# Kernel optimization log

Hardware: AMD Instinct MI355X
Metric: run time of the kernel (lower is better)

Reference implementation:

```python
import jax, jax.numpy as jnp
import numpy as np

B, N, S, D, K = 8, 8192, 2048, 256, 3
MLP = [256, 128]
EPS = 1e-5


def setup_inputs() -> dict:
    key = jax.random.key(0)
    ks = jax.random.split(key, 12)
    inp = {
        "xyz1": jax.random.normal(ks[0], (B, N, 3), dtype=jnp.float32),
        "xyz2": jax.random.normal(ks[1], (B, S, 3), dtype=jnp.float32),
        "points1": jax.random.normal(ks[2], (B, N, D), dtype=jnp.float32),
        "points2": jax.random.normal(ks[3], (B, S, D), dtype=jnp.float32),
        # relation conv: Conv2d(4 -> 1, kernel 1x1) == linear over last dim
        "rel_w": jax.random.normal(ks[4], (4,), dtype=jnp.float32) * 0.5,
        "rel_b": jnp.zeros((), dtype=jnp.float32),
        # mlp layer 0: Conv1d(2D -> 256, k=1) + BN
        "W0": jax.random.normal(ks[5], (MLP[0], 2 * D), dtype=jnp.float32) * (1.0 / np.sqrt(2 * D)),
        "b0": jnp.zeros((MLP[0],), dtype=jnp.float32),
        "g0": jnp.ones((MLP[0],), dtype=jnp.float32),
        "be0": jnp.zeros((MLP[0],), dtype=jnp.float32),
        # mlp layer 1: Conv1d(256 -> 128, k=1) + BN
        "W1": jax.random.normal(ks[6], (MLP[1], MLP[0]), dtype=jnp.float32) * (1.0 / np.sqrt(MLP[0])),
        "b1": jnp.zeros((MLP[1],), dtype=jnp.float32),
        "g1": jnp.ones((MLP[1],), dtype=jnp.float32),
        "be1": jnp.zeros((MLP[1],), dtype=jnp.float32),
    }
    return inp


def _gather(points, idx):
    # points: [B,S,C], idx: [B,N,K] -> [B,N,K,C]
    return jax.vmap(lambda p, i: p[i])(points, idx)


def _bn_relu(x, gamma, beta):
    # training-mode BatchNorm1d over [B,N,C]: stats over (B,N), biased var
    mean = jnp.mean(x, axis=(0, 1))
    var = jnp.var(x, axis=(0, 1))
    xn = (x - mean) * jax.lax.rsqrt(var + EPS)
    return jax.nn.relu(xn * gamma + beta)


def reference(xyz1, xyz2, points1, points2, rel_w, rel_b,
              W0, b0, g0, be0, W1, b1, g1, be1):
    # pairwise squared distances [B,N,S]
    d = (jnp.sum(xyz1 ** 2, -1)[:, :, None]
         + jnp.sum(xyz2 ** 2, -1)[:, None, :]
         - 2.0 * jnp.einsum('bnc,bmc->bnm', xyz1, xyz2))
    neg_d, idx = jax.lax.top_k(-d, K)          # K smallest distances
    dists = -neg_d                              # [B,N,K]

    offset = xyz1[:, :, None, :] - _gather(xyz2, idx)        # [B,N,K,3]
    rel = jnp.concatenate([dists[..., None], offset], -1)    # [B,N,K,4]
    weight = jax.nn.sigmoid(rel @ rel_w + rel_b)              # [B,N,K]

    interp = jnp.mean(_gather(points2, idx) * weight[..., None], axis=2)  # [B,N,D]
    h = jnp.concatenate([points1, interp], axis=-1)           # [B,N,2D]

    h = _bn_relu(jnp.einsum('bnc,oc->bno', h, W0) + b0, g0, be0)
    h = _bn_relu(jnp.einsum('bnc,oc->bno', h, W1) + b1, g1, be1)
    return h  # [B,N,128]
```

## Files before the change

### kernel.cpp

```cpp
#include <hip/hip_runtime.h>
#include <stdint.h>
#include <stddef.h>

#define B_   8
#define N_   8192
#define S_   2048
#define D_   256
#define M_   (B_*N_)
#define C0_  256
#define C1_  128
#define K2D_ 512
#define TS8_ 8
#define SEG8_ (S_/TS8_)
#define SWP_ 264

typedef __attribute__((ext_vector_type(8))) short short8;
typedef __attribute__((ext_vector_type(4))) float f32x4;
typedef __attribute__((ext_vector_type(2))) float f32x2;

__device__ __forceinline__ short f2bf(float f) {
  unsigned u = __float_as_uint(f);
  u += 0x7fffu + ((u >> 16) & 1u);
  return (short)(u >> 16);
}
__device__ __forceinline__ float bf2f(short s) {
  return __uint_as_float(((unsigned)(unsigned short)s) << 16);
}

__device__ __forceinline__ void cp16(const void* g, void* l) {
  __builtin_amdgcn_global_load_lds(
      (__attribute__((address_space(1))) void*)(g),
      (__attribute__((address_space(3))) void*)(l), 16, 0, 0);
}

__global__ void convw_kernel(const float* __restrict__ W0,
                             const float* __restrict__ W1,
                             const float* __restrict__ xyz2,
                             short* __restrict__ W0b, short* __restrict__ W1b,
                             float* __restrict__ xyz2p, float* __restrict__ stats) {
  int i = blockIdx.x * 256 + threadIdx.x;
  if (blockIdx.x == 0) {
    stats[threadIdx.x] = 0.f;
    stats[256 + threadIdx.x] = 0.f;
    stats[512 + threadIdx.x] = 0.f;
  }
  if (i < C0_ * K2D_) W0b[i] = f2bf(W0[i]);
  if (i < C1_ * C0_)  W1b[i] = f2bf(W1[i]);
  if (i < B_ * S_) {
    const int b = i >> 11, s = i & (S_ - 1);
    float x = xyz2[(size_t)i * 3 + 0];
    float y = xyz2[(size_t)i * 3 + 1];
    float z = xyz2[(size_t)i * 3 + 2];
    float ss = __fadd_rn(__fadd_rn(__fmul_rn(x, x), __fmul_rn(y, y)), __fmul_rn(z, z));
    float* xw = xyz2p + (size_t)b * 4 * S_;
    xw[s] = x; xw[S_ + s] = y; xw[2 * S_ + s] = z; xw[3 * S_ + s] = ss;
  }
}

__global__ __launch_bounds__(512, 8)
void topk_kernel(const float* __restrict__ xyz1, const float* __restrict__ xyz2p,
                 const float* __restrict__ relw, const float* __restrict__ relb,
                 int* __restrict__ idx_out, float* __restrict__ w_out) {
  __shared__ float cd[TS8_][64][3];
  __shared__ int   ci[TS8_][64][3];
  const int tid  = threadIdx.x;
  const int lane = tid & 63;
  const int seg  = __builtin_amdgcn_readfirstlane(tid >> 6);
  const int b    = blockIdx.x >> 7;
  const int n    = (blockIdx.x & 127) * 64 + lane;

  const float* p = xyz1 + ((size_t)b * N_ + n) * 3;
  const float ax = p[0], ay = p[1], az = p[2];
  const float s1 = __fadd_rn(__fadd_rn(__fmul_rn(ax, ax), __fmul_rn(ay, ay)), __fmul_rn(az, az));

  const float* xw = xyz2p + (size_t)b * 4 * S_;
  const f32x2* XP = (const f32x2*)(xw)           + seg * (SEG8_ / 2);
  const f32x2* YP = (const f32x2*)(xw + S_)      + seg * (SEG8_ / 2);
  const f32x2* ZP = (const f32x2*)(xw + 2 * S_)  + seg * (SEG8_ / 2);
  const f32x2* WP = (const f32x2*)(xw + 3 * S_)  + seg * (SEG8_ / 2);

  float d0 = 3.4e38f, d1 = 3.4e38f, d2 = 3.4e38f;
  int   i0 = 0, i1 = 0, i2 = 0;
  const int sbeg = seg * SEG8_;
  {
    #pragma clang fp contract(off)
    #pragma unroll 4
    for (int pr = 0; pr < SEG8_ / 2; pr++) {
      f32x2 X = XP[pr], Y = YP[pr], Z = ZP[pr], W = WP[pr];
      f32x2 t1 = ax * X;
      f32x2 t2 = ay * Y;
      f32x2 t3 = az * Z;
      f32x2 dt = (t1 + t2) + t3;
      f32x2 e  = s1 + W;
      f32x2 m  = 2.0f * dt;
      f32x2 d  = e - m;
      const float dlo = d.x, dhi = d.y;
      if (fminf(dlo, dhi) < d2) {
        const int s = sbeg + 2 * pr;
        if (dlo < d2) {
          if (dlo < d1) {
            d2 = d1; i2 = i1;
            if (dlo < d0) { d1 = d0; i1 = i0; d0 = dlo; i0 = s; }
            else          { d1 = dlo; i1 = s; }
          } else { d2 = dlo; i2 = s; }
        }
        if (dhi < d2) {
          if (dhi < d1) {
            d2 = d1; i2 = i1;
            if (dhi < d0) { d1 = d0; i1 = i0; d0 = dhi; i0 = s + 1; }
            else          { d1 = dhi; i1 = s + 1; }
          } else { d2 = dhi; i2 = s + 1; }
        }
      }
    }
  }
  cd[seg][lane][0] = d0; cd[seg][lane][1] = d1; cd[seg][lane][2] = d2;
  ci[seg][lane][0] = i0; ci[seg][lane][1] = i1; ci[seg][lane][2] = i2;
  __syncthreads();

  if (tid < 64) {
    float m0 = 3.4e38f, m1 = 3.4e38f, m2 = 3.4e38f;
    int   j0 = 0, j1 = 0, j2 = 0;
    #pragma unroll
    for (int sg = 0; sg < TS8_; sg++) {
      #pragma unroll
      for (int k = 0; k < 3; k++) {
        float d = cd[sg][tid][k];
        int   ix = ci[sg][tid][k];
        if (d < m2) {
          if (d < m1) {
            m2 = m1; j2 = j1;
            if (d < m0) { m1 = m0; j1 = j0; m0 = d; j0 = ix; }
            else        { m1 = d;  j1 = ix; }
          } else { m2 = d; j2 = ix; }
        }
      }
    }
    const float w0r = relw[0], w1r = relw[1], w2r = relw[2], w3r = relw[3], br = relb[0];
    const size_t base = ((size_t)b * N_ + n) * 3;
    float dd[3] = {m0, m1, m2};
    int   ii[3] = {j0, j1, j2};
    #pragma unroll
    for (int k = 0; k < 3; k++) {
      const int s = ii[k];
      float ox = ax - xw[s], oy = ay - xw[S_ + s], oz = az - xw[2 * S_ + s];
      float t = dd[k] * w0r + ox * w1r + oy * w2r + oz * w3r + br;
      float w = 1.0f / (1.0f + expf(-t));
      idx_out[base + k] = s;
      w_out[base + k] = w * (1.0f / 3.0f);
    }
  }
}

__global__ __launch_bounds__(256, 2)
void gemm1_kernel(const float* __restrict__ p1, const float* __restrict__ p2,
                  const int* __restrict__ idx, const float* __restrict__ wts,
                  const short* __restrict__ Bw, const float* __restrict__ bias,
                  short* __restrict__ Cb, float* __restrict__ stats) {
  __shared__ __align__(16) short sA[128 * 32];
  __shared__ __align__(16) short sB[2][256 * 32];
  const int tid = threadIdx.x;
  const int lane = tid & 63;
  const int wave = tid >> 6;
  const int wm = wave & 1;
  const int wn = wave >> 1;
  const size_t mbase = (size_t)blockIdx.x * 128;
  const int lrow = lane >> 2;
  const int lcol = (lane & 3) * 8;

  int rowg[2]; int ia[2][3]; float wa[2][3]; const float* pbase[2];
  #pragma unroll
  for (int t = 0; t < 2; t++) {
    const int row = (int)mbase + wave * 32 + t * 16 + lrow;
    rowg[t] = row;
    pbase[t] = p2 + (size_t)(row >> 13) * S_ * D_;
    ia[t][0] = idx[row * 3 + 0]; ia[t][1] = idx[row * 3 + 1]; ia[t][2] = idx[row * 3 + 2];
    wa[t][0] = wts[row * 3 + 0]; wa[t][1] = wts[row * 3 + 1]; wa[t][2] = wts[row * 3 + 2];
  }

  f32x4 acc[4][8] = {};
  float4 v[2][6];

  #define LOAD_A(K0)                                                          \
    if ((K0) < D_) {                                                          \
      _Pragma("unroll")                                                       \
      for (int t = 0; t < 2; t++) {                                           \
        const float* src = p1 + (size_t)rowg[t] * D_ + (K0) + lcol;           \
        v[t][0] = *(const float4*)src; v[t][1] = *(const float4*)(src + 4);   \
      }                                                                       \
    } else {                                                                  \
      const int c2 = (K0) - D_ + lcol;                                        \
      _Pragma("unroll")                                                       \
      for (int t = 0; t < 2; t++) {                                           \
        const float* q0 = pbase[t] + (size_t)ia[t][0] * D_ + c2;              \
        const float* q1 = pbase[t] + (size_t)ia[t][1] * D_ + c2;              \
        const float* q2 = pbase[t] + (size_t)ia[t][2] * D_ + c2;              \
        v[t][0] = *(const float4*)q0; v[t][1] = *(const float4*)(q0 + 4);     \
        v[t][2] = *(const float4*)q1; v[t][3] = *(const float4*)(q1 + 4);     \
        v[t][4] = *(const float4*)q2; v[t][5] = *(const float4*)(q2 + 4);     \
      }                                                                       \
    }

  #define STAGE_B(K0, BUF)                                                    \
    _Pragma("unroll")                                                         \
    for (int t = 0; t < 4; t++) {                                             \
      const int r = wave * 64 + t * 16;                                       \
      cp16(Bw + (size_t)(r + lrow) * K2D_ + (K0) + lcol, &sB[BUF][r * 32]);   \
    }

  LOAD_A(0);
  STAGE_B(0, 0);

  for (int k0 = 0, it = 0; k0 < K2D_; k0 += 32, it++) {
    #pragma unroll
    for (int t = 0; t < 2; t++) {
      const int r = wave * 32 + t * 16;
      float fv[8];
      if (k0 < D_) {
        fv[0] = v[t][0].x; fv[1] = v[t][0].y; fv[2] = v[t][0].z; fv[3] = v[t][0].w;
        fv[4] = v[t][1].x; fv[5] = v[t][1].y; fv[6] = v[t][1].z; fv[7] = v[t][1].w;
      } else {
        fv[0] = wa[t][0] * v[t][0].x + wa[t][1] * v[t][2].x + wa[t][2] * v[t][4].x;
        fv[1] = wa[t][0] * v[t][0].y + wa[t][1] * v[t][2].y + wa[t][2] * v[t][4].y;
        fv[2] = wa[t][0] * v[t][0].z + wa[t][1] * v[t][2].z + wa[t][2] * v[t][4].z;
        fv[3] = wa[t][0] * v[t][0].w + wa[t][1] * v[t][2].w + wa[t][2] * v[t][4].w;
        fv[4] = wa[t][0] * v[t][1].x + wa[t][1] * v[t][3].x + wa[t][2] * v[t][5].x;
        fv[5] = wa[t][0] * v[t][1].y + wa[t][1] * v[t][3].y + wa[t][2] * v[t][5].y;
        fv[6] = wa[t][0] * v[t][1].z + wa[t][1] * v[t][3].z + wa[t][2] * v[t][5].z;
        fv[7] = wa[t][0] * v[t][1].w + wa[t][1] * v[t][3].w + wa[t][2] * v[t][5].w;
      }
      short8 o;
      #pragma unroll
      for (int e = 0; e < 8; e++) o[e] = f2bf(fv[e]);
      *(short8*)&sA[(r + lrow) * 32 + lcol] = o;
    }
    __syncthreads();

    const int kn = k0 + 32;
    if (kn < K2D_) {
      STAGE_B(kn, (it + 1) & 1);
      LOAD_A(kn);
    }

    const int mr = lane & 15;
    const int ks = (lane >> 4) * 8;
    short8 af[4], bfr[8];
    #pragma unroll
    for (int i = 0; i < 4; i++) af[i]  = *(const short8*)&sA[(wm * 64 + i * 16 + mr) * 32 + ks];
    #pragma unroll
    for (int j = 0; j < 8; j++) bfr[j] = *(const short8*)&sB[it & 1][(wn * 128 + j * 16 + mr) * 32 + ks];
    #pragma unroll
    for (int i = 0; i < 4; i++)
      #pragma unroll
      for (int j = 0; j < 8; j++)
        acc[i][j] = __builtin_amdgcn_mfma_f32_16x16x32_bf16(af[i], bfr[j], acc[i][j], 0, 0, 0);
    __syncthreads();
  }
  #undef LOAD_A
  #undef STAGE_B

  const int cr = (lane >> 4) * 4;
  const int cc = lane & 15;
  float ps[8], ps2[8];
  #pragma unroll
  for (int j = 0; j < 8; j++) {
    const int col = wn * 128 + j * 16 + cc;
    const float bv = bias[col];
    float s = 0.f, s2 = 0.f;
    #pragma unroll
    for (int i = 0; i < 4; i++) {
      #pragma unroll
      for (int r = 0; r < 4; r++) {
        const float vv = acc[i][j][r];
        s += vv; s2 += vv * vv;
        const size_t row = mbase + wm * 64 + i * 16 + cr + r;
        Cb[row * C0_ + col] = f2bf(vv + bv);
      }
    }
    ps[j] = s; ps2[j] = s2;
  }
  #pragma unroll
  for (int j = 0; j < 8; j++) {
    ps[j]  += __shfl_xor(ps[j], 16);  ps[j]  += __shfl_xor(ps[j], 32);
    ps2[j] += __shfl_xor(ps2[j], 16); ps2[j] += __shfl_xor(ps2[j], 32);
  }
  float* sred = (float*)sA;
  if (wm == 1 && lane < 16) {
    #pragma unroll
    for (int j = 0; j < 8; j++) {
      const int c = wn * 128 + j * 16 + lane;
      sred[2 * c] = ps[j]; sred[2 * c + 1] = ps2[j];
    }
  }
  __syncthreads();
  if (wm == 0 && lane < 16) {
    #pragma unroll
    for (int j = 0; j < 8; j++) {
      const int c = wn * 128 + j * 16 + lane;
      atomicAdd(&stats[c],       ps[j]  + sred[2 * c]);
      atomicAdd(&stats[C0_ + c], ps2[j] + sred[2 * c + 1]);
    }
  }
}

__global__ __launch_bounds__(256, 2)
void gemm2_kernel(const short* __restrict__ A, const short* __restrict__ Bw,
                  const float* __restrict__ ssn, const float* __restrict__ bias,
                  short* __restrict__ Cb, float* __restrict__ stats) {
  __shared__ __align__(16) short sW[C1_ * SWP_];
  __shared__ float sred[3 * 256];
  const int tid = threadIdx.x;
  const int lane = tid & 63;
  const int wave = tid >> 6;
  const size_t mbase = (size_t)blockIdx.x * 128;

  #pragma unroll
  for (int i = 0; i < 16; i++) {
    const int flat = i * 256 + tid;
    const int n = flat >> 5;
    const int kb = flat & 31;
    *(short8*)&sW[n * SWP_ + kb * 8] = *(const short8*)(Bw + (size_t)flat * 8);
  }
  __syncthreads();

  f32x4 acc[2][8] = {};
  const int mr = lane & 15;
  const int ksq = (lane >> 4) * 8;

  for (int k0 = 0; k0 < C0_; k0 += 32) {
    const int kk = k0 + ksq;
    float4 sc0 = *(const float4*)(ssn + kk);
    float4 sc1 = *(const float4*)(ssn + kk + 4);
    float4 sh0 = *(const float4*)(ssn + C0_ + kk);
    float4 sh1 = *(const float4*)(ssn + C0_ + kk + 4);
    const float sc[8] = {sc0.x, sc0.y, sc0.z, sc0.w, sc1.x, sc1.y, sc1.z, sc1.w};
    const float sh[8] = {sh0.x, sh0.y, sh0.z, sh0.w, sh1.x, sh1.y, sh1.z, sh1.w};
    short8 af[2];
    #pragma unroll
    for (int i = 0; i < 2; i++) {
      const size_t row = mbase + wave * 32 + i * 16 + mr;
      short8 av = *(const short8*)(A + row * C0_ + kk);
      short8 o;
      #pragma unroll
      for (int e = 0; e < 8; e++) {
        float f = bf2f(av[e]) * sc[e] + sh[e];
        o[e] = f2bf(f > 0.f ? f : 0.f);
      }
      af[i] = o;
    }
    short8 bf8[8];
    #pragma unroll
    for (int j = 0; j < 8; j++) bf8[j] = *(const short8*)&sW[(j * 16 + mr) * SWP_ + kk];
    #pragma unroll
    for (int i = 0; i < 2; i++)
      #pragma unroll
      for (int j = 0; j < 8; j++)
        acc[i][j] = __builtin_amdgcn_mfma_f32_16x16x32_bf16(af[i], bf8[j], acc[i][j], 0, 0, 0);
  }

  const int cr = (lane >> 4) * 4;
  const int cc = lane & 15;
  float ps[8], ps2[8];
  #pragma unroll
  for (int j = 0; j < 8; j++) {
    const int col = j * 16 + cc;
    const float bv = bias[col];
    float s = 0.f, s2 = 0.f;
    #pragma unroll
    for (int i = 0; i < 2; i++) {
      #pragma unroll
      for (int r = 0; r < 4; r++) {
        const float vv = acc[i][j][r];
        s += vv; s2 += vv * vv;
        const size_t row = mbase + wave * 32 + i * 16 + cr + r;
        Cb[row * C1_ + col] = f2bf(vv + bv);
      }
    }
    ps[j] = s; ps2[j] = s2;
  }
  #pragma unroll
  for (int j = 0; j < 8; j++) {
    ps[j]  += __shfl_xor(ps[j], 16);  ps[j]  += __shfl_xor(ps[j], 32);
    ps2[j] += __shfl_xor(ps2[j], 16); ps2[j] += __shfl_xor(ps2[j], 32);
  }
  if (wave > 0 && lane < 16) {
    #pragma unroll
    for (int j = 0; j < 8; j++) {
      const int c = j * 16 + lane;
      sred[(wave - 1) * 256 + c]       = ps[j];
      sred[(wave - 1) * 256 + 128 + c] = ps2[j];
    }
  }
  __syncthreads();
  if (wave == 0 && lane < 16) {
    #pragma unroll
    for (int j = 0; j < 8; j++) {
      const int c = j * 16 + lane;
      float s  = ps[j]  + sred[c]       + sred[256 + c]       + sred[512 + c];
      float s2 = ps2[j] + sred[128 + c] + sred[256 + 128 + c] + sred[512 + 128 + c];
      atomicAdd(&stats[c],       s);
      atomicAdd(&stats[C1_ + c], s2);
    }
  }
}

__global__ void stats_final_kernel(const float* __restrict__ stats, const int C,
                                   const float* __restrict__ bias,
                                   const float* __restrict__ g, const float* __restrict__ be,
                                   float* __restrict__ ss) {
  const int c = threadIdx.x;
  if (c >= C) return;
  const float inv = 1.0f / (float)M_;
  float m0 = stats[c] * inv;
  float var = stats[C + c] * inv - m0 * m0;
  float mean = m0 + bias[c];
  float sc = g[c] * rsqrtf(var + 1e-5f);
  ss[c] = sc;
  ss[C + c] = be[c] - mean * sc;
}

__global__ __launch_bounds__(256, 1)
void norm2_kernel(const short* __restrict__ a2, const float* __restrict__ ss,
                  float* __restrict__ out) {
  const size_t t = (size_t)blockIdx.x * 256 + threadIdx.x;
  const size_t base = t * 8;
  const int c = (int)(base & (C1_ - 1));
  short8 v8 = *(const short8*)(a2 + base);
  float vv[8];
  #pragma unroll
  for (int k = 0; k < 8; k++) {
    float v = bf2f(v8[k]) * ss[c + k] + ss[C1_ + c + k];
    vv[k] = v > 0.f ? v : 0.f;
  }
  *(float4*)(out + base)     = make_float4(vv[0], vv[1], vv[2], vv[3]);
  *(float4*)(out + base + 4) = make_float4(vv[4], vv[5], vv[6], vv[7]);
}

extern "C" void kernel_launch(void* const* d_in, const int* in_sizes, int n_in,
                              void* d_out, int out_size, void* d_ws, size_t ws_size,
                              hipStream_t stream) {
  const float* xyz1 = (const float*)d_in[0];
  const float* xyz2 = (const float*)d_in[1];
  const float* pts1 = (const float*)d_in[2];
  const float* pts2 = (const float*)d_in[3];
  const float* relw = (const float*)d_in[4];
  const float* relb = (const float*)d_in[5];
  const float* W0   = (const float*)d_in[6];
  const float* b0   = (const float*)d_in[7];
  const float* g0   = (const float*)d_in[8];
  const float* be0  = (const float*)d_in[9];
  const float* W1   = (const float*)d_in[10];
  const float* b1   = (const float*)d_in[11];
  const float* g1   = (const float*)d_in[12];
  const float* be1  = (const float*)d_in[13];

  char* ws = (char*)d_ws;
  constexpr size_t IDX_OFF = 0;
  constexpr size_t WTS_OFF = IDX_OFF + (size_t)M_ * 3 * 4;
  constexpr size_t W0B_OFF = WTS_OFF + (size_t)M_ * 3 * 4;
  constexpr size_t W1B_OFF = W0B_OFF + (size_t)C0_ * K2D_ * 2;
  constexpr size_t XW_OFF  = W1B_OFF + (size_t)C1_ * C0_ * 2;
  constexpr size_t A1_OFF  = XW_OFF + (size_t)B_ * 4 * S_ * 4;
  constexpr size_t A2_OFF  = A1_OFF + (size_t)M_ * C0_ * 2;
  constexpr size_t ST_OFF  = A2_OFF + (size_t)M_ * C1_ * 2;
  constexpr size_t SS1_OFF = ST_OFF + (size_t)768 * 4;
  constexpr size_t SS2_OFF = SS1_OFF + (size_t)2 * C0_ * 4;

  int*   idx   = (int*)(ws + IDX_OFF);
  float* wts   = (float*)(ws + WTS_OFF);
  short* W0b   = (short*)(ws + W0B_OFF);
  short* W1b   = (short*)(ws + W1B_OFF);
  float* xyz2p = (float*)(ws + XW_OFF);
  short* a1    = (short*)(ws + A1_OFF);
  short* a2    = (short*)(ws + A2_OFF);
  float* st    = (float*)(ws + ST_OFF);
  float* ss1   = (float*)(ws + SS1_OFF);
  float* ss2   = (float*)(ws + SS2_OFF);
  float* outp  = (float*)d_out;

  convw_kernel<<<512, 256, 0, stream>>>(W0, W1, xyz2, W0b, W1b, xyz2p, st);
  topk_kernel<<<B_ * (N_ / 64), 512, 0, stream>>>(xyz1, xyz2p, relw, relb, idx, wts);

  gemm1_kernel<<<M_ / 128, 256, 0, stream>>>(pts1, pts2, idx, wts, W0b, b0, a1, st);
  stats_final_kernel<<<1, 256, 0, stream>>>(st, C0_, b0, g0, be0, ss1);

  gemm2_kernel<<<M_ / 128, 256, 0, stream>>>(a1, W1b, ss1, b1, a2, st + 512);
  stats_final_kernel<<<1, 128, 0, stream>>>(st + 512, C1_, b1, g1, be1, ss2);
  norm2_kernel<<<(size_t)M_ * C1_ / 8 / 256, 256, 0, stream>>>(a2, ss2, outp);
}
```

Measured before the change: 292.1 us.

## Restructure gemm1 so each wave owns full-width rows with direct-register operands

The first GEMM is rebuilt so that each wave computes 32 rows across all 256 output columns. The A fragment (points1 or the weighted gather of points2) is built directly in registers as the MFMA operand, and the B weights are read straight from global memory each k-step, with no LDS staging and no per-iteration barriers. The bf16 output is staged through a padded LDS tile and written back as coalesced 16-byte rows, and the BN statistics are reduced across all four waves. The aim is to remove the LDS round trip and __syncthreads per k-step. The trade-offs are more global or L2 traffic for weights, since every wave reloads the full B slice, and a much larger LDS footprint that may limit occupancy.

```diff
diff --git a/kernel.cpp b/kernel.cpp
--- a/kernel.cpp
+++ b/kernel.cpp
@@ -13,6 +13,7 @@
 #define TS8_ 8
 #define SEG8_ (S_/TS8_)
 #define SWP_ 264
+#define SWC_ 268
 
 typedef __attribute__((ext_vector_type(8))) short short8;
 typedef __attribute__((ext_vector_type(4))) float f32x4;
@@ -157,149 +158,141 @@
                   const int* __restrict__ idx, const float* __restrict__ wts,
                   const short* __restrict__ Bw, const float* __restrict__ bias,
                   short* __restrict__ Cb, float* __restrict__ stats) {
-  __shared__ __align__(16) short sA[128 * 32];
-  __shared__ __align__(16) short sB[2][256 * 32];
-  const int tid = threadIdx.x;
+  __shared__ __align__(16) short sC[128 * SWC_];
+  __shared__ float sred[3][2][C0_];
+  const int tid  = threadIdx.x;
   const int lane = tid & 63;
   const int wave = tid >> 6;
-  const int wm = wave & 1;
-  const int wn = wave >> 1;
-  const size_t mbase = (size_t)blockIdx.x * 128;
-  const int lrow = lane >> 2;
-  const int lcol = (lane & 3) * 8;
+  const int mr = lane & 15;
+  const int kq = (lane >> 4) * 8;
+  const int r0 = blockIdx.x * 128 + wave * 32;
 
   int rowg[2]; int ia[2][3]; float wa[2][3]; const float* pbase[2];
   #pragma unroll
   for (int t = 0; t < 2; t++) {
-    const int row = (int)mbase + wave * 32 + t * 16 + lrow;
+    const int row = r0 + t * 16 + mr;
     rowg[t] = row;
     pbase[t] = p2 + (size_t)(row >> 13) * S_ * D_;
     ia[t][0] = idx[row * 3 + 0]; ia[t][1] = idx[row * 3 + 1]; ia[t][2] = idx[row * 3 + 2];
     wa[t][0] = wts[row * 3 + 0]; wa[t][1] = wts[row * 3 + 1]; wa[t][2] = wts[row * 3 + 2];
   }
 
-  f32x4 acc[4][8] = {};
-  float4 v[2][6];
+  f32x4 acc[2][16] = {};
+  float4 ar[2][6];
 
   #define LOAD_A(K0)                                                          \
     if ((K0) < D_) {                                                          \
       _Pragma("unroll")                                                       \
       for (int t = 0; t < 2; t++) {                                           \
-        const float* src = p1 + (size_t)rowg[t] * D_ + (K0) + lcol;           \
-        v[t][0] = *(const float4*)src; v[t][1] = *(const float4*)(src + 4);   \
+        const float* src = p1 + (size_t)rowg[t] * D_ + (K0) + kq;             \
+        ar[t][0] = *(const float4*)src; ar[t][1] = *(const float4*)(src + 4); \
       }                                                                       \
     } else {                                                                  \
-      const int c2 = (K0) - D_ + lcol;                                        \
+      const int c2 = (K0) - D_ + kq;                                          \
       _Pragma("unroll")                                                       \
       for (int t = 0; t < 2; t++) {                                           \
         const float* q0 = pbase[t] + (size_t)ia[t][0] * D_ + c2;              \
         const float* q1 = pbase[t] + (size_t)ia[t][1] * D_ + c2;              \
         const float* q2 = pbase[t] + (size_t)ia[t][2] * D_ + c2;              \
-        v[t][0] = *(const float4*)q0; v[t][1] = *(const float4*)(q0 + 4);     \
-        v[t][2] = *(const float4*)q1; v[t][3] = *(const float4*)(q1 + 4);     \
-        v[t][4] = *(const float4*)q2; v[t][5] = *(const float4*)(q2 + 4);     \
+        ar[t][0] = *(const float4*)q0; ar[t][1] = *(const float4*)(q0 + 4);   \
+        ar[t][2] = *(const float4*)q1; ar[t][3] = *(const float4*)(q1 + 4);   \
+        ar[t][4] = *(const float4*)q2; ar[t][5] = *(const float4*)(q2 + 4);   \
       }                                                                       \
     }
 
-  #define STAGE_B(K0, BUF)                                                    \
-    _Pragma("unroll")                                                         \
-    for (int t = 0; t < 4; t++) {                                             \
-      const int r = wave * 64 + t * 16;                                       \
-      cp16(Bw + (size_t)(r + lrow) * K2D_ + (K0) + lcol, &sB[BUF][r * 32]);   \
-    }
-
   LOAD_A(0);
-  STAGE_B(0, 0);
-
-  for (int k0 = 0, it = 0; k0 < K2D_; k0 += 32, it++) {
-    #pragma unroll
-    for (int t = 0; t < 2; t++) {
-      const int r = wave * 32 + t * 16;
-      float fv[8];
-      if (k0 < D_) {
-        fv[0] = v[t][0].x; fv[1] = v[t][0].y; fv[2] = v[t][0].z; fv[3] = v[t][0].w;
-        fv[4] = v[t][1].x; fv[5] = v[t][1].y; fv[6] = v[t][1].z; fv[7] = v[t][1].w;
-      } else {
-        fv[0] = wa[t][0] * v[t][0].x + wa[t][1] * v[t][2].x + wa[t][2] * v[t][4].x;
-        fv[1] = wa[t][0] * v[t][0].y + wa[t][1] * v[t][2].y + wa[t][2] * v[t][4].y;
-        fv[2] = wa[t][0] * v[t][0].z + wa[t][1] * v[t][2].z + wa[t][2] * v[t][4].z;
-        fv[3] = wa[t][0] * v[t][0].w + wa[t][1] * v[t][2].w + wa[t][2] * v[t][4].w;
-        fv[4] = wa[t][0] * v[t][1].x + wa[t][1] * v[t][3].x + wa[t][2] * v[t][5].x;
-        fv[5] = wa[t][0] * v[t][1].y + wa[t][1] * v[t][3].y + wa[t][2] * v[t][5].y;
-        fv[6] = wa[t][0] * v[t][1].z + wa[t][1] * v[t][3].z + wa[t][2] * v[t][5].z;
-        fv[7] = wa[t][0] * v[t][1].w + wa[t][1] * v[t][3].w + wa[t][2] * v[t][5].w;
-      }
-      short8 o;
-      #pragma unroll
-      for (int e = 0; e < 8; e++) o[e] = f2bf(fv[e]);
-      *(short8*)&sA[(r + lrow) * 32 + lcol] = o;
-    }
-    __syncthreads();
-
+
+  #pragma unroll 1
+  for (int k0 = 0; k0 < K2D_; k0 += 32) {
+    short8 af[2];
+    if (k0 < D_) {
+      #pragma unroll
+      for (int t = 0; t < 2; t++) {
+        float fv[8] = {ar[t][0].x, ar[t][0].y, ar[t][0].z, ar[t][0].w,
+                       ar[t][1].x, ar[t][1].y, ar[t][1].z, ar[t][1].w};
+        short8 o;
+        #pragma unroll
+        for (int e = 0; e < 8; e++) o[e] = f2bf(fv[e]);
+        af[t] = o;
+      }
+    } else {
+      #pragma unroll
+      for (int t = 0; t < 2; t++) {
+        float fv[8];
+        fv[0] = wa[t][0] * ar[t][0].x + wa[t][1] * ar[t][2].x + wa[t][2] * ar[t][4].x;
+        fv[1] = wa[t][0] * ar[t][0].y + wa[t][1] * ar[t][2].y + wa[t][2] * ar[t][4].y;
+        fv[2] = wa[t][0] * ar[t][0].z + wa[t][1] * ar[t][2].z + wa[t][2] * ar[t][4].z;
+        fv[3] = wa[t][0] * ar[t][0].w + wa[t][1] * ar[t][2].w + wa[t][2] * ar[t][4].w;
+        fv[4] = wa[t][0] * ar[t][1].x + wa[t][1] * ar[t][3].x + wa[t][2] * ar[t][5].x;
+        fv[5] = wa[t][0] * ar[t][1].y + wa[t][1] * ar[t][3].y + wa[t][2] * ar[t][5].y;
+        fv[6] = wa[t][0] * ar[t][1].z + wa[t][1] * ar[t][3].z + wa[t][2] * ar[t][5].z;
+        fv[7] = wa[t][0] * ar[t][1].w + wa[t][1] * ar[t][3].w + wa[t][2] * ar[t][5].w;
+        short8 o;
+        #pragma unroll
+        for (int e = 0; e < 8; e++) o[e] = f2bf(fv[e]);
+        af[t] = o;
+      }
+    }
     const int kn = k0 + 32;
-    if (kn < K2D_) {
-      STAGE_B(kn, (it + 1) & 1);
-      LOAD_A(kn);
-    }
-
-    const int mr = lane & 15;
-    const int ks = (lane >> 4) * 8;
-    short8 af[4], bfr[8];
-    #pragma unroll
-    for (int i = 0; i < 4; i++) af[i]  = *(const short8*)&sA[(wm * 64 + i * 16 + mr) * 32 + ks];
-    #pragma unroll
-    for (int j = 0; j < 8; j++) bfr[j] = *(const short8*)&sB[it & 1][(wn * 128 + j * 16 + mr) * 32 + ks];
-    #pragma unroll
-    for (int i = 0; i < 4; i++)
-      #pragma unroll
-      for (int j = 0; j < 8; j++)
-        acc[i][j] = __builtin_amdgcn_mfma_f32_16x16x32_bf16(af[i], bfr[j], acc[i][j], 0, 0, 0);
-    __syncthreads();
+    if (kn < K2D_) { LOAD_A(kn); }
+
+    #pragma unroll
+    for (int j = 0; j < 16; j++) {
+      short8 bf = *(const short8*)(Bw + (size_t)(j * 16 + mr) * K2D_ + k0 + kq);
+      acc[0][j] = __builtin_amdgcn_mfma_f32_16x16x32_bf16(af[0], bf, acc[0][j], 0, 0, 0);
+      acc[1][j] = __builtin_amdgcn_mfma_f32_16x16x32_bf16(af[1], bf, acc[1][j], 0, 0, 0);
+    }
   }
   #undef LOAD_A
-  #undef STAGE_B
 
   const int cr = (lane >> 4) * 4;
   const int cc = lane & 15;
-  float ps[8], ps2[8];
-  #pragma unroll
-  for (int j = 0; j < 8; j++) {
-    const int col = wn * 128 + j * 16 + cc;
+  float ps[16], ps2[16];
+  #pragma unroll
+  for (int j = 0; j < 16; j++) {
+    const int col = j * 16 + cc;
     const float bv = bias[col];
     float s = 0.f, s2 = 0.f;
     #pragma unroll
-    for (int i = 0; i < 4; i++) {
+    for (int t = 0; t < 2; t++) {
       #pragma unroll
       for (int r = 0; r < 4; r++) {
-        const float vv = acc[i][j][r];
-        s += vv; s2 += vv * vv;
-        const size_t row = mbase + wm * 64 + i * 16 + cr + r;
-        Cb[row * C0_ + col] = f2bf(vv + bv);
+        const float v = acc[t][j][r];
+        s += v; s2 += v * v;
+        sC[(wave * 32 + t * 16 + cr + r) * SWC_ + col] = f2bf(v + bv);
       }
     }
     ps[j] = s; ps2[j] = s2;
   }
   #pragma unroll
-  for (int j = 0; j < 8; j++) {
+  for (int j = 0; j < 16; j++) {
     ps[j]  += __shfl_xor(ps[j], 16);  ps[j]  += __shfl_xor(ps[j], 32);
     ps2[j] += __shfl_xor(ps2[j], 16); ps2[j] += __shfl_xor(ps2[j], 32);
   }
-  float* sred = (float*)sA;
-  if (wm == 1 && lane < 16) {
-    #pragma unroll
-    for (int j = 0; j < 8; j++) {
-      const int c = wn * 128 + j * 16 + lane;
-      sred[2 * c] = ps[j]; sred[2 * c + 1] = ps2[j];
+  if (wave > 0 && lane < 16) {
+    #pragma unroll
+    for (int j = 0; j < 16; j++) {
+      const int c = j * 16 + lane;
+      sred[wave - 1][0][c] = ps[j];
+      sred[wave - 1][1][c] = ps2[j];
     }
   }
   __syncthreads();
-  if (wm == 0 && lane < 16) {
-    #pragma unroll
-    for (int j = 0; j < 8; j++) {
-      const int c = wn * 128 + j * 16 + lane;
-      atomicAdd(&stats[c],       ps[j]  + sred[2 * c]);
-      atomicAdd(&stats[C0_ + c], ps2[j] + sred[2 * c + 1]);
-    }
+  if (wave == 0 && lane < 16) {
+    #pragma unroll
+    for (int j = 0; j < 16; j++) {
+      const int c = j * 16 + lane;
+      atomicAdd(&stats[c],       ps[j]  + sred[0][0][c] + sred[1][0][c] + sred[2][0][c]);
+      atomicAdd(&stats[C0_ + c], ps2[j] + sred[0][1][c] + sred[1][1][c] + sred[2][1][c]);
+    }
+  }
+  #pragma unroll
+  for (int t2 = 0; t2 < 16; t2++) {
+    const int flat = t2 * 256 + tid;
+    const int rr = flat >> 5;
+    const int ch = flat & 31;
+    short8 vv = *(short8*)&sC[rr * SWC_ + ch * 8];
+    *(short8*)(Cb + ((size_t)blockIdx.x * 128 + rr) * C0_ + ch * 8) = vv;
   }
 }
 
```

Measured after the change: 334.2 us. +14.4%, slower.
